# Performance work log

Measured on AMD Instinct MI355X. Metric: run time of the kernel, lower is better.

Reference implementation:

```python
import jax, jax.numpy as jnp
import numpy as np

B, L, D = 2, 2048, 1024
NUM_HEADS = 16
HEAD_DIM = D // NUM_HEADS


def setup_inputs() -> dict:
    key = jax.random.key(0)
    k1, k2 = jax.random.split(key)
    x = jax.random.normal(k1, (B, L, D), dtype=jnp.float32)
    # torch Linear(input_dim, 3*output_dim, bias=False); store as [in, 3*out] for x @ W
    W_qkv = jax.random.normal(k2, (D, 3 * D), dtype=jnp.float32) * (1.0 / np.sqrt(D))
    return {"x": x, "W_qkv": W_qkv}


def reference(x, W_qkv):
    b, l, d = x.shape
    h, hd = NUM_HEADS, HEAD_DIM
    qkv = x @ W_qkv                                  # [B, L, 3*D]
    qkv = qkv.reshape(b, l, 3, h, hd)
    q = jnp.transpose(qkv[:, :, 0], (0, 2, 1, 3))    # [B, H, L, hd]
    k = jnp.transpose(qkv[:, :, 1], (0, 2, 1, 3))
    v = jnp.transpose(qkv[:, :, 2], (0, 2, 1, 3))
    scale = 1.0 / jnp.sqrt(jnp.asarray(hd, dtype=x.dtype))
    scores = jnp.einsum('bhqd,bhkd->bhqk', q, k) * scale   # [B, H, L, L]
    causal = jnp.triu(jnp.ones((l, l), dtype=bool), k=1)   # True above diagonal -> masked
    scores = jnp.where(causal, -jnp.inf, scores)
    attn = jax.nn.softmax(scores, axis=-1)
    # dropout p=0.0 -> identity (eval mode)
    out = jnp.einsum('bhqk,bhkd->bhqd', attn, v)            # [B, H, L, hd]
    out = jnp.transpose(out, (0, 2, 1, 3)).reshape(b, l, h * hd)
    return out
```

## Files before the change

### kernel.cpp

```cpp
#include <hip/hip_runtime.h>
#include <hip/hip_bf16.h>
#include <math.h>

#define NB_L 2048
#define GM 4096
#define GN 3072
#define GK 1024
#define NROWS 65536
#define SCALE_L2E 0.180336880f

typedef float  f4v __attribute__((ext_vector_type(4)));
typedef short  s4v __attribute__((ext_vector_type(4)));
typedef short  s8v __attribute__((ext_vector_type(8)));

#define MFMA_16x16x32(a, b, c) __builtin_amdgcn_mfma_f32_16x16x32_bf16((a), (b), (c), 0, 0, 0)
#define MFMA_16x16x16(a, b, c) __builtin_amdgcn_mfma_f32_16x16x16bf16_1k((a), (b), (c), 0, 0, 0)

static __device__ __forceinline__ unsigned int bfpk(float a, float b) {
    __hip_bfloat162 h = __float22bfloat162_rn(float2{a, b});
    union { __hip_bfloat162 h2; unsigned int u; } cv; cv.h2 = h; return cv.u;
}
static __device__ __forceinline__ unsigned short bf1(float a) {
    union { __hip_bfloat16 h; unsigned short u; } cv; cv.h = __float2bfloat16(a); return cv.u;
}
static __device__ __forceinline__ float bf2f(unsigned short u) {
    union { unsigned int u; float f; } cv; cv.u = ((unsigned int)u) << 16; return cv.f;
}

static __device__ __forceinline__ void gl_lds16(const ushort* g, ushort* l) {
#if defined(__has_builtin) && __has_builtin(__builtin_amdgcn_global_load_lds)
    __builtin_amdgcn_global_load_lds((const __attribute__((address_space(1))) void*)g,
                                     (__attribute__((address_space(3))) void*)l, 16, 0, 0);
#else
    *(s8v*)l = *(const s8v*)g;
#endif
}

__global__ __launch_bounds__(256) void conv_x(const float* __restrict__ X, ushort* __restrict__ Xb) {
    const int i = blockIdx.x * 256 + threadIdx.x;
    const float4 f0 = ((const float4*)X)[2 * i];
    const float4 f1 = ((const float4*)X)[2 * i + 1];
    uint4 u;
    u.x = bfpk(f0.x, f0.y); u.y = bfpk(f0.z, f0.w);
    u.z = bfpk(f1.x, f1.y); u.w = bfpk(f1.z, f1.w);
    ((uint4*)Xb)[i] = u;
}

__global__ __launch_bounds__(256) void conv_wt(const float* __restrict__ W, ushort* __restrict__ Wt) {
    __shared__ __align__(16) ushort T[64][72];
    const int t = threadIdx.x;
    const int k0 = blockIdx.x * 64, n0 = blockIdx.y * 64;
    {
        const int kr = t >> 2, nc0 = (t & 3) * 16;
        const float* src = W + (size_t)(k0 + kr) * GN + n0 + nc0;
#pragma unroll
        for (int u = 0; u < 4; ++u) {
            const float4 v = *(const float4*)(src + 4 * u);
            T[nc0 + 4 * u + 0][kr] = bf1(v.x);
            T[nc0 + 4 * u + 1][kr] = bf1(v.y);
            T[nc0 + 4 * u + 2][kr] = bf1(v.z);
            T[nc0 + 4 * u + 3][kr] = bf1(v.w);
        }
    }
    __syncthreads();
    {
        const int nr = t >> 2, kc0 = (t & 3) * 16;
        ushort* dst = Wt + (size_t)(n0 + nr) * GK + k0 + kc0;
        *(s8v*)dst       = *(const s8v*)&T[nr][kc0];
        *(s8v*)(dst + 8) = *(const s8v*)&T[nr][kc0 + 8];
    }
}

__global__ __launch_bounds__(256) void qkv_gemm_bf16(
    const ushort* __restrict__ Xb, const ushort* __restrict__ Wt, ushort* __restrict__ Qkv)
{
    __shared__ __align__(16) ushort As[4][128][8];
    __shared__ __align__(16) ushort Bs[4][128][8];
    const int tid = threadIdx.x;
    const int row0 = blockIdx.y * 128, col0 = blockIdx.x * 128;
    const int mA = tid & 127, k2a = tid >> 7;
    const int lane = tid & 63, w = tid >> 6;
    const int wr = w >> 1, wc = w & 1, lq = lane & 15, quad = lane >> 4;

    f4v acc[4][4];
#pragma unroll
    for (int g = 0; g < 4; ++g)
#pragma unroll
        for (int j = 0; j < 4; ++j) acc[g][j] = 0.f;

    const ushort* gA = Xb + (size_t)(row0 + mA) * GK + k2a * 8;
    const ushort* gB = Wt + (size_t)(col0 + mA) * GK + k2a * 8;
    ushort* lA0 = &As[k2a][mA][0];
    ushort* lA1 = &As[k2a + 2][mA][0];
    ushort* lB0 = &Bs[k2a][mA][0];
    ushort* lB1 = &Bs[k2a + 2][mA][0];

    for (int it = 0; it < 32; ++it) {
        const int k0 = it * 32;
        __syncthreads();
        gl_lds16(gA + k0, lA0);
        gl_lds16(gA + k0 + 16, lA1);
        gl_lds16(gB + k0, lB0);
        gl_lds16(gB + k0 + 16, lB1);
        __syncthreads();

        s8v af[4], bfr[4];
#pragma unroll
        for (int g = 0; g < 4; ++g) af[g]  = *(const s8v*)&As[quad][wr * 64 + g * 16 + lq][0];
#pragma unroll
        for (int j = 0; j < 4; ++j) bfr[j] = *(const s8v*)&Bs[quad][wc * 64 + j * 16 + lq][0];
#pragma unroll
        for (int g = 0; g < 4; ++g)
#pragma unroll
            for (int j = 0; j < 4; ++j)
                acc[g][j] = MFMA_16x16x32(af[g], bfr[j], acc[g][j]);
    }

    const float qscale = (col0 < 1024) ? SCALE_L2E : 1.0f;
#pragma unroll
    for (int g = 0; g < 4; ++g)
#pragma unroll
        for (int j = 0; j < 4; ++j) {
            const int col = col0 + wc * 64 + j * 16 + lq;
#pragma unroll
            for (int r = 0; r < 4; ++r) {
                const int row = row0 + wr * 64 + g * 16 + quad * 4 + r;
                Qkv[(size_t)row * GN + col] = bf1(acc[g][j][r] * qscale);
            }
        }
}

__global__ __launch_bounds__(256, 4) void attn_bf16(
    const ushort* __restrict__ Qkv, ushort* __restrict__ Opart, float* __restrict__ Lp)
{
    __shared__ __align__(16) ushort Ks[8][64][8];
    __shared__ __align__(16) ushort Vt[64][72];

    const int x = blockIdx.x;
    const int bh = x & 31;
    const int qlow = (x >> 5) & 7;
    const int s = (x >> 8) & 1;
    const int x9 = (x >> 9) & 1;
    const int qt = x9 ? (15 - qlow) : qlow;
    const int h = bh & 15, b = bh >> 4;

    const int tid = threadIdx.x;
    const int w = tid >> 6, lane = tid & 63;
    const int lq = lane & 15, quad = lane >> 4;
    const int boff = b * NB_L;
    const int qrow_base = qt * 128 + w * 32;
    const int diag = 2 * qt + (w >> 1);

    s8v qf[2][2];
#pragma unroll
    for (int qg = 0; qg < 2; ++qg)
#pragma unroll
        for (int sb = 0; sb < 2; ++sb)
            qf[qg][sb] = *(const s8v*)(Qkv + (size_t)(boff + qrow_base + qg * 16 + lq) * GN
                                       + h * 64 + sb * 32 + quad * 8);

    f4v o[4][2];
#pragma unroll
    for (int dg = 0; dg < 4; ++dg)
#pragma unroll
        for (int qg = 0; qg < 2; ++qg) o[dg][qg] = 0.f;
    float l_s[2] = {0.f, 0.f};

    const int kt_lo = s ? (qt + 1) : 0;
    const int kt_hi = s ? (2 * qt + 1) : qt;

    const int pr  = tid >> 2;
    const int dc0 = (tid & 3) * 16, dc4 = tid & 3;
    const int vcol = (2 * pr + 16 * dc4) & 63;
    const int t2 = tid & 127;
    const int krow_s = t2 >> 1, g0 = (t2 & 1) * 4;

    s8v preg[4];
    if (tid < 128) {
        const ushort* vp = Qkv + (size_t)(boff + kt_lo * 64 + 2 * pr) * GN + 2048 + h * 64 + dc0;
        preg[0] = *(const s8v*)vp;        preg[1] = *(const s8v*)(vp + 8);
        preg[2] = *(const s8v*)(vp + GN); preg[3] = *(const s8v*)(vp + GN + 8);
    } else {
        const ushort* kp = Qkv + (size_t)(boff + kt_lo * 64 + krow_s) * GN + 1024 + h * 64 + g0 * 8;
#pragma unroll
        for (int i = 0; i < 4; ++i) preg[i] = *(const s8v*)(kp + 8 * i);
    }

    for (int kt = kt_lo; kt <= kt_hi; ++kt) {
        __syncthreads();
        if (tid < 128) {
#pragma unroll
            for (int j = 0; j < 16; ++j) {
                const unsigned short lo = (unsigned short)((j < 8) ? preg[0][j] : preg[1][j - 8]);
                const unsigned short hi = (unsigned short)((j < 8) ? preg[2][j] : preg[3][j - 8]);
                *(unsigned int*)&Vt[dc0 + j][vcol] = (unsigned int)lo | ((unsigned int)hi << 16);
            }
        } else {
#pragma unroll
            for (int i = 0; i < 4; ++i)
                *(s8v*)&Ks[g0 + i][krow_s][0] = preg[i];
        }
        __syncthreads();

        if (kt < kt_hi) {
            if (tid < 128) {
                const ushort* vp = Qkv + (size_t)(boff + (kt + 1) * 64 + 2 * pr) * GN + 2048 + h * 64 + dc0;
                preg[0] = *(const s8v*)vp;        preg[1] = *(const s8v*)(vp + 8);
                preg[2] = *(const s8v*)(vp + GN); preg[3] = *(const s8v*)(vp + GN + 8);
            } else {
                const ushort* kp = Qkv + (size_t)(boff + (kt + 1) * 64 + krow_s) * GN + 1024 + h * 64 + g0 * 8;
#pragma unroll
                for (int i = 0; i < 4; ++i) preg[i] = *(const s8v*)(kp + 8 * i);
            }
        }

        if (kt <= diag) {
            f4v st[4][2];
#pragma unroll
            for (int kg = 0; kg < 4; ++kg)
#pragma unroll
                for (int qg = 0; qg < 2; ++qg) st[kg][qg] = 0.f;
#pragma unroll
            for (int kg = 0; kg < 4; ++kg) {
#pragma unroll
                for (int sb = 0; sb < 2; ++sb) {
                    const s8v af = *(const s8v*)&Ks[sb * 4 + quad][kg * 16 + lq][0];
#pragma unroll
                    for (int qg = 0; qg < 2; ++qg)
                        st[kg][qg] = MFMA_16x16x32(af, qf[qg][sb], st[kg][qg]);
                }
            }
            if (kt == diag) {
#pragma unroll
                for (int kg = 0; kg < 4; ++kg)
#pragma unroll
                    for (int qg = 0; qg < 2; ++qg) {
                        const int qrow = qrow_base + qg * 16 + lq;
#pragma unroll
                        for (int r = 0; r < 4; ++r)
                            if (kt * 64 + kg * 16 + quad * 4 + r > qrow)
                                st[kg][qg][r] = -INFINITY;
                    }
            }
#pragma unroll
            for (int qg = 0; qg < 2; ++qg) {
                float sum = 0.f;
#pragma unroll
                for (int kg = 0; kg < 4; ++kg)
#pragma unroll
                    for (int r = 0; r < 4; ++r) {
                        const float p = exp2f(st[kg][qg][r]);
                        st[kg][qg][r] = p;
                        sum += p;
                    }
                sum += __shfl_xor(sum, 16);
                sum += __shfl_xor(sum, 32);
                l_s[qg] += sum;
            }
#pragma unroll
            for (int ks = 0; ks < 4; ++ks) {
                s4v pb[2];
#pragma unroll
                for (int qg = 0; qg < 2; ++qg) {
                    union { s4v v; uint2 u; } c;
                    c.u.x = bfpk(st[ks][qg][0], st[ks][qg][1]);
                    c.u.y = bfpk(st[ks][qg][2], st[ks][qg][3]);
                    pb[qg] = c.v;
                }
#pragma unroll
                for (int dg = 0; dg < 4; ++dg) {
                    const s4v va = *(const s4v*)&Vt[dg * 16 + lq][((ks + dg) & 3) * 16 + quad * 4];
#pragma unroll
                    for (int qg = 0; qg < 2; ++qg)
                        o[dg][qg] = MFMA_16x16x16(va, pb[qg], o[dg][qg]);
                }
            }
        }
    }

#pragma unroll
    for (int qg = 0; qg < 2; ++qg) {
        const size_t prow = (size_t)(s * 32 + bh) * 2048 + qrow_base + qg * 16 + lq;
#pragma unroll
        for (int dg = 0; dg < 4; ++dg) {
            const int d = dg * 16 + quad * 4;
            uint2 u;
            u.x = bfpk(o[dg][qg][0], o[dg][qg][1]);
            u.y = bfpk(o[dg][qg][2], o[dg][qg][3]);
            *(uint2*)&Opart[prow * 64 + d] = u;
        }
        if (quad == 0) Lp[prow] = l_s[qg];
    }
}

__global__ __launch_bounds__(256) void attn_combine(
    const ushort* __restrict__ Opart, const float* __restrict__ Lp, float* __restrict__ Out)
{
    const int id = blockIdx.x * 256 + threadIdx.x;
    const int row = id >> 4, c4 = (id & 15) * 4;
    const float l0 = Lp[row], l1 = Lp[row + NROWS];
    const float inv = 1.0f / (l0 + l1);

    const s4v a = *(const s4v*)&Opart[(size_t)row * 64 + c4];
    const s4v c = *(const s4v*)&Opart[(size_t)(row + NROWS) * 64 + c4];
    float4 v;
    v.x = (bf2f((unsigned short)a[0]) + bf2f((unsigned short)c[0])) * inv;
    v.y = (bf2f((unsigned short)a[1]) + bf2f((unsigned short)c[1])) * inv;
    v.z = (bf2f((unsigned short)a[2]) + bf2f((unsigned short)c[2])) * inv;
    v.w = (bf2f((unsigned short)a[3]) + bf2f((unsigned short)c[3])) * inv;

    const int bh = row >> 11, qrow = row & 2047;
    const int b = bh >> 4, h = bh & 15;
    *(float4*)(Out + ((size_t)(b * 2048 + qrow)) * 1024 + h * 64 + c4) = v;
}

extern "C" void kernel_launch(void* const* d_in, const int* in_sizes, int n_in,
                              void* d_out, int out_size, void* d_ws, size_t ws_size,
                              hipStream_t stream)
{
    const float* x  = (const float*)d_in[0];
    const float* wq = (const float*)d_in[1];
    float* out = (float*)d_out;

    ushort* wsp  = (ushort*)d_ws;
    ushort* qkvb = wsp;
    ushort* xb   = wsp + (size_t)GM * GN;
    ushort* wt   = xb + (size_t)GM * GK;
    ushort* opart = wsp + (size_t)GM * GN;
    float*  lp    = (float*)(opart + (size_t)2 * NROWS * 64);

    conv_x<<<GM * GK / (256 * 8), 256, 0, stream>>>(x, xb);
    conv_wt<<<dim3(GK / 64, GN / 64), 256, 0, stream>>>(wq, wt);
    qkv_gemm_bf16<<<dim3(GN / 128, GM / 128), 256, 0, stream>>>(xb, wt, qkvb);
    attn_bf16<<<1024, 256, 0, stream>>>(qkvb, opart, lp);
    attn_combine<<<NROWS * 16 / 256, 256, 0, stream>>>(opart, lp, out);
}
```

Baseline: 202.6 us.

## Double-buffer LDS tiles in QKV GEMM and attention to drop a barrier

The QKV GEMM now keeps two LDS stage buffers and issues the async global-to-LDS loads for the next K-slice before running the MFMAs on the current slice. This removes the second barrier per iteration. The attention kernel also double-buffers its K and V^T tiles. Each iteration stores the prefetched registers into one buffer and computes on the tile written the step before, with a peeled final compute. The aim is to overlap LDS fills and global loads with MFMA work and halve the barriers per step, at the cost of twice the shared memory, which could limit occupancy.

```diff
diff --git a/kernel.cpp b/kernel.cpp
--- a/kernel.cpp
+++ b/kernel.cpp
@@ -74,8 +74,8 @@
 __global__ __launch_bounds__(256) void qkv_gemm_bf16(
     const ushort* __restrict__ Xb, const ushort* __restrict__ Wt, ushort* __restrict__ Qkv)
 {
-    __shared__ __align__(16) ushort As[4][128][8];
-    __shared__ __align__(16) ushort Bs[4][128][8];
+    __shared__ __align__(16) ushort As[2][4][128][8];
+    __shared__ __align__(16) ushort Bs[2][4][128][8];
     const int tid = threadIdx.x;
     const int row0 = blockIdx.y * 128, col0 = blockIdx.x * 128;
     const int mA = tid & 127, k2a = tid >> 7;
@@ -90,25 +90,28 @@
 
     const ushort* gA = Xb + (size_t)(row0 + mA) * GK + k2a * 8;
     const ushort* gB = Wt + (size_t)(col0 + mA) * GK + k2a * 8;
-    ushort* lA0 = &As[k2a][mA][0];
-    ushort* lA1 = &As[k2a + 2][mA][0];
-    ushort* lB0 = &Bs[k2a][mA][0];
-    ushort* lB1 = &Bs[k2a + 2][mA][0];
+
+    gl_lds16(gA,      &As[0][k2a][mA][0]);
+    gl_lds16(gA + 16, &As[0][k2a + 2][mA][0]);
+    gl_lds16(gB,      &Bs[0][k2a][mA][0]);
+    gl_lds16(gB + 16, &Bs[0][k2a + 2][mA][0]);
 
     for (int it = 0; it < 32; ++it) {
-        const int k0 = it * 32;
+        const int cur = it & 1, nxt = cur ^ 1;
         __syncthreads();
-        gl_lds16(gA + k0, lA0);
-        gl_lds16(gA + k0 + 16, lA1);
-        gl_lds16(gB + k0, lB0);
-        gl_lds16(gB + k0 + 16, lB1);
-        __syncthreads();
+        if (it + 1 < 32) {
+            const int k0 = (it + 1) * 32;
+            gl_lds16(gA + k0,      &As[nxt][k2a][mA][0]);
+            gl_lds16(gA + k0 + 16, &As[nxt][k2a + 2][mA][0]);
+            gl_lds16(gB + k0,      &Bs[nxt][k2a][mA][0]);
+            gl_lds16(gB + k0 + 16, &Bs[nxt][k2a + 2][mA][0]);
+        }
 
         s8v af[4], bfr[4];
 #pragma unroll
-        for (int g = 0; g < 4; ++g) af[g]  = *(const s8v*)&As[quad][wr * 64 + g * 16 + lq][0];
-#pragma unroll
-        for (int j = 0; j < 4; ++j) bfr[j] = *(const s8v*)&Bs[quad][wc * 64 + j * 16 + lq][0];
+        for (int g = 0; g < 4; ++g) af[g]  = *(const s8v*)&As[cur][quad][wr * 64 + g * 16 + lq][0];
+#pragma unroll
+        for (int j = 0; j < 4; ++j) bfr[j] = *(const s8v*)&Bs[cur][quad][wc * 64 + j * 16 + lq][0];
 #pragma unroll
         for (int g = 0; g < 4; ++g)
 #pragma unroll
@@ -133,8 +136,8 @@
 __global__ __launch_bounds__(256, 4) void attn_bf16(
     const ushort* __restrict__ Qkv, ushort* __restrict__ Opart, float* __restrict__ Lp)
 {
-    __shared__ __align__(16) ushort Ks[8][64][8];
-    __shared__ __align__(16) ushort Vt[64][72];
+    __shared__ __align__(16) ushort Ks[2][8][64][8];
+    __shared__ __align__(16) ushort Vt[2][64][72];
 
     const int x = blockIdx.x;
     const int bh = x & 31;
@@ -168,12 +171,77 @@
 
     const int kt_lo = s ? (qt + 1) : 0;
     const int kt_hi = s ? (2 * qt + 1) : qt;
+    const int niter = kt_hi - kt_lo + 1;
 
     const int pr  = tid >> 2;
     const int dc0 = (tid & 3) * 16, dc4 = tid & 3;
     const int vcol = (2 * pr + 16 * dc4) & 63;
     const int t2 = tid & 127;
     const int krow_s = t2 >> 1, g0 = (t2 & 1) * 4;
+
+    auto compute = [&](int ktc, int bufi) {
+        if (ktc > diag) return;
+        f4v st[4][2];
+#pragma unroll
+        for (int kg = 0; kg < 4; ++kg)
+#pragma unroll
+            for (int qg = 0; qg < 2; ++qg) st[kg][qg] = 0.f;
+#pragma unroll
+        for (int kg = 0; kg < 4; ++kg) {
+#pragma unroll
+            for (int sb = 0; sb < 2; ++sb) {
+                const s8v af = *(const s8v*)&Ks[bufi][sb * 4 + quad][kg * 16 + lq][0];
+#pragma unroll
+                for (int qg = 0; qg < 2; ++qg)
+                    st[kg][qg] = MFMA_16x16x32(af, qf[qg][sb], st[kg][qg]);
+            }
+        }
+        if (ktc == diag) {
+#pragma unroll
+            for (int kg = 0; kg < 4; ++kg)
+#pragma unroll
+                for (int qg = 0; qg < 2; ++qg) {
+                    const int qrow = qrow_base + qg * 16 + lq;
+#pragma unroll
+                    for (int r = 0; r < 4; ++r)
+                        if (ktc * 64 + kg * 16 + quad * 4 + r > qrow)
+                            st[kg][qg][r] = -INFINITY;
+                }
+        }
+#pragma unroll
+        for (int qg = 0; qg < 2; ++qg) {
+            float sum = 0.f;
+#pragma unroll
+            for (int kg = 0; kg < 4; ++kg)
+#pragma unroll
+                for (int r = 0; r < 4; ++r) {
+                    const float p = exp2f(st[kg][qg][r]);
+                    st[kg][qg][r] = p;
+                    sum += p;
+                }
+            sum += __shfl_xor(sum, 16);
+            sum += __shfl_xor(sum, 32);
+            l_s[qg] += sum;
+        }
+#pragma unroll
+        for (int ks = 0; ks < 4; ++ks) {
+            s4v pb[2];
+#pragma unroll
+            for (int qg = 0; qg < 2; ++qg) {
+                union { s4v v; uint2 u; } c;
+                c.u.x = bfpk(st[ks][qg][0], st[ks][qg][1]);
+                c.u.y = bfpk(st[ks][qg][2], st[ks][qg][3]);
+                pb[qg] = c.v;
+            }
+#pragma unroll
+            for (int dg = 0; dg < 4; ++dg) {
+                const s4v va = *(const s4v*)&Vt[bufi][dg * 16 + lq][((ks + dg) & 3) * 16 + quad * 4];
+#pragma unroll
+                for (int qg = 0; qg < 2; ++qg)
+                    o[dg][qg] = MFMA_16x16x16(va, pb[qg], o[dg][qg]);
+            }
+        }
+    };
 
     s8v preg[4];
     if (tid < 128) {
@@ -186,97 +254,37 @@
         for (int i = 0; i < 4; ++i) preg[i] = *(const s8v*)(kp + 8 * i);
     }
 
-    for (int kt = kt_lo; kt <= kt_hi; ++kt) {
+    for (int i = 0; i < niter; ++i) {
+        const int wb = i & 1;
         __syncthreads();
         if (tid < 128) {
 #pragma unroll
             for (int j = 0; j < 16; ++j) {
                 const unsigned short lo = (unsigned short)((j < 8) ? preg[0][j] : preg[1][j - 8]);
                 const unsigned short hi = (unsigned short)((j < 8) ? preg[2][j] : preg[3][j - 8]);
-                *(unsigned int*)&Vt[dc0 + j][vcol] = (unsigned int)lo | ((unsigned int)hi << 16);
+                *(unsigned int*)&Vt[wb][dc0 + j][vcol] = (unsigned int)lo | ((unsigned int)hi << 16);
             }
         } else {
 #pragma unroll
-            for (int i = 0; i < 4; ++i)
-                *(s8v*)&Ks[g0 + i][krow_s][0] = preg[i];
-        }
-        __syncthreads();
-
-        if (kt < kt_hi) {
+            for (int i2 = 0; i2 < 4; ++i2)
+                *(s8v*)&Ks[wb][g0 + i2][krow_s][0] = preg[i2];
+        }
+        if (i + 1 < niter) {
+            const int ktn = kt_lo + i + 1;
             if (tid < 128) {
-                const ushort* vp = Qkv + (size_t)(boff + (kt + 1) * 64 + 2 * pr) * GN + 2048 + h * 64 + dc0;
+                const ushort* vp = Qkv + (size_t)(boff + ktn * 64 + 2 * pr) * GN + 2048 + h * 64 + dc0;
                 preg[0] = *(const s8v*)vp;        preg[1] = *(const s8v*)(vp + 8);
                 preg[2] = *(const s8v*)(vp + GN); preg[3] = *(const s8v*)(vp + GN + 8);
             } else {
-                const ushort* kp = Qkv + (size_t)(boff + (kt + 1) * 64 + krow_s) * GN + 1024 + h * 64 + g0 * 8;
-#pragma unroll
-                for (int i = 0; i < 4; ++i) preg[i] = *(const s8v*)(kp + 8 * i);
-            }
-        }
-
-        if (kt <= diag) {
-            f4v st[4][2];
-#pragma unroll
-            for (int kg = 0; kg < 4; ++kg)
-#pragma unroll
-                for (int qg = 0; qg < 2; ++qg) st[kg][qg] = 0.f;
-#pragma unroll
-            for (int kg = 0; kg < 4; ++kg) {
-#pragma unroll
-                for (int sb = 0; sb < 2; ++sb) {
-                    const s8v af = *(const s8v*)&Ks[sb * 4 + quad][kg * 16 + lq][0];
-#pragma unroll
-                    for (int qg = 0; qg < 2; ++qg)
-                        st[kg][qg] = MFMA_16x16x32(af, qf[qg][sb], st[kg][qg]);
-                }
-            }
-            if (kt == diag) {
-#pragma unroll
-                for (int kg = 0; kg < 4; ++kg)
-#pragma unroll
-                    for (int qg = 0; qg < 2; ++qg) {
-                        const int qrow = qrow_base + qg * 16 + lq;
-#pragma unroll
-                        for (int r = 0; r < 4; ++r)
-                            if (kt * 64 + kg * 16 + quad * 4 + r > qrow)
-                                st[kg][qg][r] = -INFINITY;
-                    }
-            }
-#pragma unroll
-            for (int qg = 0; qg < 2; ++qg) {
-                float sum = 0.f;
-#pragma unroll
-                for (int kg = 0; kg < 4; ++kg)
-#pragma unroll
-                    for (int r = 0; r < 4; ++r) {
-                        const float p = exp2f(st[kg][qg][r]);
-                        st[kg][qg][r] = p;
-                        sum += p;
-                    }
-                sum += __shfl_xor(sum, 16);
-                sum += __shfl_xor(sum, 32);
-                l_s[qg] += sum;
-            }
-#pragma unroll
-            for (int ks = 0; ks < 4; ++ks) {
-                s4v pb[2];
-#pragma unroll
-                for (int qg = 0; qg < 2; ++qg) {
-                    union { s4v v; uint2 u; } c;
-                    c.u.x = bfpk(st[ks][qg][0], st[ks][qg][1]);
-                    c.u.y = bfpk(st[ks][qg][2], st[ks][qg][3]);
-                    pb[qg] = c.v;
-                }
-#pragma unroll
-                for (int dg = 0; dg < 4; ++dg) {
-                    const s4v va = *(const s4v*)&Vt[dg * 16 + lq][((ks + dg) & 3) * 16 + quad * 4];
-#pragma unroll
-                    for (int qg = 0; qg < 2; ++qg)
-                        o[dg][qg] = MFMA_16x16x16(va, pb[qg], o[dg][qg]);
-                }
-            }
-        }
-    }
+                const ushort* kp = Qkv + (size_t)(boff + ktn * 64 + krow_s) * GN + 1024 + h * 64 + g0 * 8;
+#pragma unroll
+                for (int i2 = 0; i2 < 4; ++i2) preg[i2] = *(const s8v*)(kp + 8 * i2);
+            }
+        }
+        if (i > 0) compute(kt_lo + i - 1, wb ^ 1);
+    }
+    __syncthreads();
+    compute(kt_hi, (niter - 1) & 1);
 
 #pragma unroll
     for (int qg = 0; qg < 2; ++qg) {
```

After: 200.1 us. Within noise of the previous version (-1.3%).
